# Performance work log

Measured on AMD Instinct MI355X. Metric: run time of the kernel, lower is better.

## Reference

```python
import jax, jax.numpy as jnp
import numpy as np

NEG_SLOPE = 0.01  # F.leaky_relu default


def gcn_conv(x, src, dst, norm, W, b, n_nodes):
    """PyG-style GCNConv: h = x @ W; out[i] = sum_{(j->i)} norm_e * h[j] + b.
    src/dst/norm already include self-loops and symmetric D^-1/2 A D^-1/2 weights."""
    h = x @ W                                   # [N, out]
    msgs = h[src] * norm[:, None]               # [E+N, out] gather
    out = jax.ops.segment_sum(msgs, dst, num_segments=n_nodes)  # scatter-add
    return out + b


def _build_norm(edge_idx, n_nodes):
    """Add self-loops and compute symmetric GCN normalization coefficients."""
    loops = jnp.arange(n_nodes, dtype=edge_idx.dtype)
    src = jnp.concatenate([edge_idx[0], loops])
    dst = jnp.concatenate([edge_idx[1], loops])
    deg = jax.ops.segment_sum(jnp.ones_like(dst, dtype=jnp.float32), dst,
                              num_segments=n_nodes)
    dinv = jnp.where(deg > 0, jax.lax.rsqrt(jnp.maximum(deg, 1.0)), 0.0)
    norm = dinv[src] * dinv[dst]
    return src, dst, norm


def setup_inputs() -> dict:
    key = jax.random.key(0)
    k = jax.random.split(key, 8)
    N, E, nfeat, nhid = 50000, 800000, 64, 64
    x = jax.random.normal(k[0], (N, nfeat), dtype=jnp.float32)
    edge_idx = jax.random.randint(k[1], (2, E), 0, N, dtype=jnp.int32)
    # inverted dropout mask, p=0.5 -> values in {0, 2}
    drop_mask = (jax.random.uniform(k[2], (N, nhid)) >= 0.5).astype(jnp.float32) * 2.0
    # glorot-style GCNConv weights + zero bias (PyG defaults)
    s1 = (6.0 / (nfeat + nhid)) ** 0.5
    s2 = (6.0 / (nhid + nhid // 2)) ** 0.5
    W1 = jax.random.uniform(k[3], (nfeat, nhid), minval=-s1, maxval=s1, dtype=jnp.float32)
    b1 = jnp.zeros((nhid,), dtype=jnp.float32)
    W2 = jax.random.uniform(k[4], (nhid, nhid // 2), minval=-s2, maxval=s2, dtype=jnp.float32)
    b2 = jnp.zeros((nhid // 2,), dtype=jnp.float32)
    return {"x": x, "edge_idx": edge_idx, "drop_mask": drop_mask,
            "W1": W1, "b1": b1, "W2": W2, "b2": b2}


def reference(x, edge_idx, drop_mask, W1, b1, W2, b2):
    n_nodes = x.shape[0]
    src, dst, norm = _build_norm(edge_idx, n_nodes)
    h = jax.nn.leaky_relu(gcn_conv(x, src, dst, norm, W1, b1, n_nodes), NEG_SLOPE)
    h = h * drop_mask  # F.dropout(p=0.5) with precomputed inverted mask
    out = jax.nn.leaky_relu(gcn_conv(h, src, dst, norm, W2, b2, n_nodes), NEG_SLOPE)
    return out
```

## Files before the change

kernel.cpp:

```cpp
#include <hip/hip_runtime.h>
#include <hip/hip_fp16.h>

#define NEG_SLOPE 0.01f
typedef unsigned int uint;
typedef unsigned short u16;

#define NBK 256
#define CHUNK 4096
#define KPT 16
#define GROWS 16

__device__ __forceinline__ float wbits(uint rec) {
    u16 b = (u16)(rec >> 16);
    __half h;
    *reinterpret_cast<u16*>(&h) = b;
    return __half2float(h);
}

__device__ __forceinline__ void acc8(uint4 v, float w, float* a) {
    float2 f;
    f = __half22float2(*reinterpret_cast<__half2*>(&v.x)); a[0] = fmaf(f.x, w, a[0]); a[1] = fmaf(f.y, w, a[1]);
    f = __half22float2(*reinterpret_cast<__half2*>(&v.y)); a[2] = fmaf(f.x, w, a[2]); a[3] = fmaf(f.y, w, a[3]);
    f = __half22float2(*reinterpret_cast<__half2*>(&v.z)); a[4] = fmaf(f.x, w, a[4]); a[5] = fmaf(f.y, w, a[5]);
    f = __half22float2(*reinterpret_cast<__half2*>(&v.w)); a[6] = fmaf(f.x, w, a[6]); a[7] = fmaf(f.y, w, a[7]);
}

__device__ __forceinline__ void unpack8(uint4 v, float* s) {
    float2 f;
    f = __half22float2(*reinterpret_cast<__half2*>(&v.x)); s[0] = f.x; s[1] = f.y;
    f = __half22float2(*reinterpret_cast<__half2*>(&v.y)); s[2] = f.x; s[3] = f.y;
    f = __half22float2(*reinterpret_cast<__half2*>(&v.z)); s[4] = f.x; s[5] = f.y;
    f = __half22float2(*reinterpret_cast<__half2*>(&v.w)); s[6] = f.x; s[7] = f.y;
}

__global__ __launch_bounds__(256) void bucket_hist(const int* __restrict__ dst,
                                                   uint* __restrict__ hist,
                                                   int E) {
    __shared__ uint lh[NBK];
    int t = threadIdx.x;
    lh[t] = 0u;
    __syncthreads();
    int base = blockIdx.x * CHUNK;
#pragma unroll
    for (int r = 0; r < 4; ++r) {
        int e4 = base + r * 1024 + t * 4;
        if (e4 + 3 < E) {
            int4 d = *(const int4*)(dst + e4);
            atomicAdd(&lh[((uint)d.x) >> 8], 1u);
            atomicAdd(&lh[((uint)d.y) >> 8], 1u);
            atomicAdd(&lh[((uint)d.z) >> 8], 1u);
            atomicAdd(&lh[((uint)d.w) >> 8], 1u);
        } else {
            for (int e = e4; e < E && e < e4 + 4; ++e)
                atomicAdd(&lh[((uint)dst[e]) >> 8], 1u);
        }
    }
    __syncthreads();
    hist[(size_t)blockIdx.x * NBK + t] = lh[t];
}

__global__ __launch_bounds__(256) void scan_hist(uint* __restrict__ hist,
                                                 uint* __restrict__ buckTotal,
                                                 int nchunks) {
    __shared__ uint lds[256];
    int b = blockIdx.x;
    int t = threadIdx.x;
    uint carry = 0;
    for (int c0 = 0; c0 < nchunks; c0 += 256) {
        int c = c0 + t;
        uint v = (c < nchunks) ? hist[(size_t)c * NBK + b] : 0u;
        lds[t] = v;
        __syncthreads();
        for (int off = 1; off < 256; off <<= 1) {
            uint u = (t >= off) ? lds[t - off] : 0u;
            __syncthreads();
            lds[t] += u;
            __syncthreads();
        }
        uint incl = lds[t];
        if (c < nchunks) hist[(size_t)c * NBK + b] = carry + incl - v;
        uint tot = lds[255];
        __syncthreads();
        carry += tot;
    }
    if (t == 0) buckTotal[b] = carry;
}

__global__ __launch_bounds__(256) void partition_edges(const int* __restrict__ src,
                                                       const int* __restrict__ dst,
                                                       const uint* __restrict__ hist,
                                                       const uint* __restrict__ buckTotal,
                                                       uint* __restrict__ staging,
                                                       int E) {
    __shared__ uint lh[NBK];
    __shared__ uint sc[NBK];
    __shared__ uint runbase[NBK];
    int t = threadIdx.x;
    lh[t] = 0u;
    uint tot = buckTotal[t];
    sc[t] = tot;
    __syncthreads();
    for (int off = 1; off < NBK; off <<= 1) {
        uint u = (t >= off) ? sc[t - off] : 0u;
        __syncthreads();
        sc[t] += u;
        __syncthreads();
    }
    int base = blockIdx.x * CHUNK;
    uint rec[KPT], rb[KPT], rk[KPT];
#pragma unroll
    for (int r = 0; r < 4; ++r) {
        int e4 = base + r * 1024 + t * 4;
        if (e4 + 3 < E) {
            int4 s = *(const int4*)(src + e4);
            int4 d = *(const int4*)(dst + e4);
            int k = r * 4;
            rb[k + 0] = ((uint)d.x) >> 8; rec[k + 0] = (uint)s.x | (((uint)d.x & 255u) << 16);
            rb[k + 1] = ((uint)d.y) >> 8; rec[k + 1] = (uint)s.y | (((uint)d.y & 255u) << 16);
            rb[k + 2] = ((uint)d.z) >> 8; rec[k + 2] = (uint)s.z | (((uint)d.z & 255u) << 16);
            rb[k + 3] = ((uint)d.w) >> 8; rec[k + 3] = (uint)s.w | (((uint)d.w & 255u) << 16);
            rk[k + 0] = atomicAdd(&lh[rb[k + 0]], 1u);
            rk[k + 1] = atomicAdd(&lh[rb[k + 1]], 1u);
            rk[k + 2] = atomicAdd(&lh[rb[k + 2]], 1u);
            rk[k + 3] = atomicAdd(&lh[rb[k + 3]], 1u);
        } else {
            for (int j = 0; j < 4; ++j) {
                int e = e4 + j;
                int k = r * 4 + j;
                if (e < E) {
                    uint s = (uint)src[e], d = (uint)dst[e];
                    rb[k] = d >> 8;
                    rec[k] = s | ((d & 255u) << 16);
                    rk[k] = atomicAdd(&lh[rb[k]], 1u);
                } else rb[k] = 0xFFFFFFFFu;
            }
        }
    }
    __syncthreads();
    runbase[t] = (sc[t] - tot) + hist[(size_t)blockIdx.x * NBK + t];
    __syncthreads();
#pragma unroll
    for (int k = 0; k < KPT; ++k)
        if (rb[k] != 0xFFFFFFFFu)
            staging[runbase[rb[k]] + rk[k]] = rec[k];
}

__global__ __launch_bounds__(256) void build_csr(const uint* __restrict__ staging,
                                                 const uint* __restrict__ buckTotal,
                                                 u16* __restrict__ srcIdx,
                                                 uint* __restrict__ offs,
                                                 float* __restrict__ dinv,
                                                 int N, int nbuck) {
    __shared__ uint nh[256];
    __shared__ uint nstart[256];
    __shared__ u16 rankbuf[8192];
    __shared__ u16 outbuf[8192];
    int b = blockIdx.x;
    int t = threadIdx.x;
    uint tot = buckTotal[t];
    nstart[t] = tot;
    __syncthreads();
    for (int off = 1; off < NBK; off <<= 1) {
        uint u = (t >= off) ? nstart[t - off] : 0u;
        __syncthreads();
        nstart[t] += u;
        __syncthreads();
    }
    uint endb = nstart[b];
    uint base = endb - buckTotal[b];
    __syncthreads();
    uint T = endb - base;
    nh[t] = 0u;
    __syncthreads();
    for (uint i = t; i < T; i += 256) {
        uint rec = staging[base + i];
        rankbuf[i] = (u16)atomicAdd(&nh[(rec >> 16) & 255u], 1u);
    }
    __syncthreads();
    uint deg = nh[t];
    nstart[t] = deg;
    __syncthreads();
    for (int off = 1; off < 256; off <<= 1) {
        uint u = (t >= off) ? nstart[t - off] : 0u;
        __syncthreads();
        nstart[t] += u;
        __syncthreads();
    }
    uint excl = nstart[t] - deg;
    __syncthreads();
    nstart[t] = excl;
    __syncthreads();
    for (uint i = t; i < T; i += 256) {
        uint rec = staging[base + i];
        outbuf[nstart[(rec >> 16) & 255u] + rankbuf[i]] = (u16)(rec & 0xFFFFu);
    }
    __syncthreads();
    for (uint i = t; i < T; i += 256) srcIdx[base + i] = outbuf[i];
    int node = b * 256 + t;
    if (node < N) {
        offs[node] = base + excl;
        dinv[node] = rsqrtf((float)(deg + 1u));
    }
    if (b == nbuck - 1 && t == 0) offs[N] = endb;
}

__global__ __launch_bounds__(256) void fill_pack(const u16* __restrict__ srcIdx,
                                                 const float* __restrict__ dinv,
                                                 uint* __restrict__ packed, int E) {
    int i4 = (blockIdx.x * 256 + threadIdx.x) * 4;
    if (i4 + 3 < E) {
        ushort4 s = *(const ushort4*)(srcIdx + i4);
        uint4 o;
        __half h0 = __float2half(dinv[s.x]);
        __half h1 = __float2half(dinv[s.y]);
        __half h2 = __float2half(dinv[s.z]);
        __half h3 = __float2half(dinv[s.w]);
        o.x = (uint)s.x | ((uint)*reinterpret_cast<u16*>(&h0) << 16);
        o.y = (uint)s.y | ((uint)*reinterpret_cast<u16*>(&h1) << 16);
        o.z = (uint)s.z | ((uint)*reinterpret_cast<u16*>(&h2) << 16);
        o.w = (uint)s.w | ((uint)*reinterpret_cast<u16*>(&h3) << 16);
        *(uint4*)(packed + i4) = o;
    } else {
        for (int i = i4; i < E; ++i) {
            __half h = __float2half(dinv[srcIdx[i]]);
            packed[i] = (uint)srcIdx[i] | ((uint)*reinterpret_cast<u16*>(&h) << 16);
        }
    }
}

__global__ __launch_bounds__(256) void gemm64x64(const float* __restrict__ X,
                                                 const float* __restrict__ W,
                                                 __half* __restrict__ H, int N) {
    int lane = threadIdx.x & 63;
    int wv = threadIdx.x >> 6;
    float wc[64];
#pragma unroll
    for (int k = 0; k < 64; ++k) wc[k] = W[k * 64 + lane];
    int rowBase = (blockIdx.x * 4 + wv) * GROWS;
    for (int g = 0; g < GROWS; g += 4) {
        int r0 = __builtin_amdgcn_readfirstlane(rowBase + g);
        if (r0 >= N) return;
        int e1 = min(r0 + 1, N - 1), e2 = min(r0 + 2, N - 1), e3 = min(r0 + 3, N - 1);
        const float* x0 = X + (size_t)r0 * 64;
        const float* x1 = X + (size_t)e1 * 64;
        const float* x2 = X + (size_t)e2 * 64;
        const float* x3 = X + (size_t)e3 * 64;
        float a0 = 0.f, a1 = 0.f, a2 = 0.f, a3 = 0.f;
        float b0 = 0.f, b1 = 0.f, b2 = 0.f, b3 = 0.f;
#pragma unroll
        for (int k = 0; k < 64; k += 2) {
            a0 = fmaf(x0[k], wc[k], a0); b0 = fmaf(x0[k + 1], wc[k + 1], b0);
            a1 = fmaf(x1[k], wc[k], a1); b1 = fmaf(x1[k + 1], wc[k + 1], b1);
            a2 = fmaf(x2[k], wc[k], a2); b2 = fmaf(x2[k + 1], wc[k + 1], b2);
            a3 = fmaf(x3[k], wc[k], a3); b3 = fmaf(x3[k + 1], wc[k + 1], b3);
        }
        H[(size_t)r0 * 64 + lane] = __float2half(a0 + b0);
        if (r0 + 1 < N) H[(size_t)(r0 + 1) * 64 + lane] = __float2half(a1 + b1);
        if (r0 + 2 < N) H[(size_t)(r0 + 2) * 64 + lane] = __float2half(a2 + b2);
        if (r0 + 3 < N) H[(size_t)(r0 + 3) * 64 + lane] = __float2half(a3 + b3);
    }
}

__global__ __launch_bounds__(256) void gemm64x32(const __half* __restrict__ Xh,
                                                 const float* __restrict__ W,
                                                 __half* __restrict__ H, int N) {
    int lane = threadIdx.x & 63;
    int col = lane & 31;
    int wv = threadIdx.x >> 6;
    float wc[64];
#pragma unroll
    for (int k = 0; k < 64; ++k) wc[k] = W[k * 32 + col];
    int rowBase = (blockIdx.x * 4 + wv) * GROWS;
    for (int g = 0; g < GROWS; g += 4) {
        int r0 = __builtin_amdgcn_readfirstlane(rowBase + g);
        if (r0 >= N) return;
        int e1 = min(r0 + 1, N - 1), e2 = min(r0 + 2, N - 1), e3 = min(r0 + 3, N - 1);
        const uint* x0 = (const uint*)(Xh + (size_t)r0 * 64);
        const uint* x1 = (const uint*)(Xh + (size_t)e1 * 64);
        const uint* x2 = (const uint*)(Xh + (size_t)e2 * 64);
        const uint* x3 = (const uint*)(Xh + (size_t)e3 * 64);
        float a0 = 0.f, a1 = 0.f, a2 = 0.f, a3 = 0.f;
        float b0 = 0.f, b1 = 0.f, b2 = 0.f, b3 = 0.f;
#pragma unroll
        for (int kk = 0; kk < 32; ++kk) {
            uint u0 = x0[kk], u1 = x1[kk], u2 = x2[kk], u3 = x3[kk];
            float2 f0 = __half22float2(*reinterpret_cast<__half2*>(&u0));
            float2 f1 = __half22float2(*reinterpret_cast<__half2*>(&u1));
            float2 f2 = __half22float2(*reinterpret_cast<__half2*>(&u2));
            float2 f3 = __half22float2(*reinterpret_cast<__half2*>(&u3));
            a0 = fmaf(f0.x, wc[2 * kk], a0); b0 = fmaf(f0.y, wc[2 * kk + 1], b0);
            a1 = fmaf(f1.x, wc[2 * kk], a1); b1 = fmaf(f1.y, wc[2 * kk + 1], b1);
            a2 = fmaf(f2.x, wc[2 * kk], a2); b2 = fmaf(f2.y, wc[2 * kk + 1], b2);
            a3 = fmaf(f3.x, wc[2 * kk], a3); b3 = fmaf(f3.y, wc[2 * kk + 1], b3);
        }
        if (lane < 32) {
            H[(size_t)r0 * 32 + col] = __float2half(a0 + b0);
            if (r0 + 1 < N) H[(size_t)(r0 + 1) * 32 + col] = __float2half(a1 + b1);
            if (r0 + 2 < N) H[(size_t)(r0 + 2) * 32 + col] = __float2half(a2 + b2);
            if (r0 + 3 < N) H[(size_t)(r0 + 3) * 32 + col] = __float2half(a3 + b3);
        }
    }
}

__global__ __launch_bounds__(256) void agg1(const __half* __restrict__ h,
                                            const uint* __restrict__ offs,
                                            const uint* __restrict__ packed,
                                            const float* __restrict__ dinv,
                                            const float* __restrict__ b,
                                            const float* __restrict__ mask,
                                            __half* __restrict__ outp, int N) {
    int node = blockIdx.x * 4 + (threadIdx.x >> 6);
    if (node >= N) return;
    int lane = threadIdx.x & 63;
    int r = lane >> 3;
    int q = lane & 7;
    const uint4* h16 = (const uint4*)h;
    uint beg = offs[node], end = offs[node + 1];
    float a[8] = {0.f, 0.f, 0.f, 0.f, 0.f, 0.f, 0.f, 0.f};
    uint p = beg + (uint)r;
    for (; p + 24 < end; p += 32) {
        uint e0 = packed[p], e1 = packed[p + 8], e2 = packed[p + 16], e3 = packed[p + 24];
        uint4 v0 = h16[(size_t)(e0 & 0xFFFFu) * 8 + q];
        uint4 v1 = h16[(size_t)(e1 & 0xFFFFu) * 8 + q];
        uint4 v2 = h16[(size_t)(e2 & 0xFFFFu) * 8 + q];
        uint4 v3 = h16[(size_t)(e3 & 0xFFFFu) * 8 + q];
        acc8(v0, wbits(e0), a);
        acc8(v1, wbits(e1), a);
        acc8(v2, wbits(e2), a);
        acc8(v3, wbits(e3), a);
    }
    for (; p < end; p += 8) {
        uint e0 = packed[p];
        uint4 v0 = h16[(size_t)(e0 & 0xFFFFu) * 8 + q];
        acc8(v0, wbits(e0), a);
    }
#pragma unroll
    for (int i = 0; i < 8; ++i) {
        a[i] += __shfl_xor(a[i], 8, 64);
        a[i] += __shfl_xor(a[i], 16, 64);
        a[i] += __shfl_xor(a[i], 32, 64);
    }
    if (r == 0) {
        float dv = dinv[node];
        float dv2 = dv * dv;
        float s[8];
        unpack8(h16[(size_t)node * 8 + q], s);
        float4 bv0 = ((const float4*)b)[q * 2];
        float4 bv1 = ((const float4*)b)[q * 2 + 1];
        float4 mv0 = ((const float4*)mask)[(size_t)node * 16 + q * 2];
        float4 mv1 = ((const float4*)mask)[(size_t)node * 16 + q * 2 + 1];
        float bb[8] = {bv0.x, bv0.y, bv0.z, bv0.w, bv1.x, bv1.y, bv1.z, bv1.w};
        float mm[8] = {mv0.x, mv0.y, mv0.z, mv0.w, mv1.x, mv1.y, mv1.z, mv1.w};
        uint4 o;
        uint* op = (uint*)&o;
#pragma unroll
        for (int i = 0; i < 4; ++i) {
            float v0 = a[2 * i] * dv + s[2 * i] * dv2 + bb[2 * i];
            float v1 = a[2 * i + 1] * dv + s[2 * i + 1] * dv2 + bb[2 * i + 1];
            v0 = (v0 > 0.f) ? v0 : NEG_SLOPE * v0;
            v1 = (v1 > 0.f) ? v1 : NEG_SLOPE * v1;
            v0 *= mm[2 * i]; v1 *= mm[2 * i + 1];
            __half2 hh = __floats2half2_rn(v0, v1);
            op[i] = *reinterpret_cast<uint*>(&hh);
        }
        ((uint4*)outp)[(size_t)node * 8 + q] = o;
    }
}

__global__ __launch_bounds__(256) void agg2(const __half* __restrict__ h,
                                            const uint* __restrict__ offs,
                                            const uint* __restrict__ packed,
                                            const float* __restrict__ dinv,
                                            const float* __restrict__ b,
                                            float* __restrict__ outp, int N) {
    int node = blockIdx.x * 4 + (threadIdx.x >> 6);
    if (node >= N) return;
    int lane = threadIdx.x & 63;
    int r = lane >> 2;
    int q = lane & 3;
    const uint4* h8 = (const uint4*)h;
    uint beg = offs[node], end = offs[node + 1];
    float a[8] = {0.f, 0.f, 0.f, 0.f, 0.f, 0.f, 0.f, 0.f};
    uint p = beg + (uint)r;
    for (; p + 16 < end; p += 32) {
        uint e0 = packed[p], e1 = packed[p + 16];
        uint4 v0 = h8[(size_t)(e0 & 0xFFFFu) * 4 + q];
        uint4 v1 = h8[(size_t)(e1 & 0xFFFFu) * 4 + q];
        acc8(v0, wbits(e0), a);
        acc8(v1, wbits(e1), a);
    }
    for (; p < end; p += 16) {
        uint e0 = packed[p];
        uint4 v0 = h8[(size_t)(e0 & 0xFFFFu) * 4 + q];
        acc8(v0, wbits(e0), a);
    }
#pragma unroll
    for (int i = 0; i < 8; ++i) {
        a[i] += __shfl_xor(a[i], 4, 64);
        a[i] += __shfl_xor(a[i], 8, 64);
        a[i] += __shfl_xor(a[i], 16, 64);
        a[i] += __shfl_xor(a[i], 32, 64);
    }
    if (r == 0) {
        float dv = dinv[node];
        float dv2 = dv * dv;
        float s[8];
        unpack8(h8[(size_t)node * 4 + q], s);
        float4 bv0 = ((const float4*)b)[q * 2];
        float4 bv1 = ((const float4*)b)[q * 2 + 1];
        float bb[8] = {bv0.x, bv0.y, bv0.z, bv0.w, bv1.x, bv1.y, bv1.z, bv1.w};
        float o[8];
#pragma unroll
        for (int i = 0; i < 8; ++i) {
            float v = a[i] * dv + s[i] * dv2 + bb[i];
            o[i] = (v > 0.f) ? v : NEG_SLOPE * v;
        }
        float4* outv = (float4*)outp;
        outv[(size_t)node * 8 + q * 2]     = make_float4(o[0], o[1], o[2], o[3]);
        outv[(size_t)node * 8 + q * 2 + 1] = make_float4(o[4], o[5], o[6], o[7]);
    }
}

extern "C" void kernel_launch(void* const* d_in, const int* in_sizes, int n_in,
                              void* d_out, int out_size, void* d_ws, size_t ws_size,
                              hipStream_t stream) {
    const float* x    = (const float*)d_in[0];
    const int*   ei   = (const int*)d_in[1];
    const float* mask = (const float*)d_in[2];
    const float* W1   = (const float*)d_in[3];
    const float* b1   = (const float*)d_in[4];
    const float* W2   = (const float*)d_in[5];
    const float* b2   = (const float*)d_in[6];
    float* out = (float*)d_out;

    const int N = in_sizes[0] / 64;
    const int E = in_sizes[1] / 2;
    const int* src = ei;
    const int* dst = ei + E;

    const int nbuck  = (N + 255) >> 8;
    const int chunks = (E + CHUNK - 1) / CHUNK;
    const int gblocks = (N + 4 * GROWS - 1) / (4 * GROWS);

    char* w = (char*)d_ws;
    uint*  hist      = (uint*)w;    w += (size_t)chunks * NBK * 4;
    uint*  buckTotal = (uint*)w;    w += NBK * 4;
    w = (char*)(((size_t)w + 15) & ~15ull);
    uint*  offs      = (uint*)w;    w += (size_t)(N + 1) * 4;
    w = (char*)(((size_t)w + 15) & ~15ull);
    float* dinv      = (float*)w;   w += (size_t)N * 4;
    uint*  staging   = (uint*)w;    w += (size_t)E * 4;
    u16*   srcIdx    = (u16*)w;     w += (((size_t)E * 2 + 15) & ~15ull);
    uint*  packed    = (uint*)w;    w += (size_t)E * 4;
    __half* h1       = (__half*)w;  w += (size_t)N * 64 * 2;
    __half* hpost    = (__half*)w;  w += (size_t)N * 64 * 2;
    __half* h2       = h1;

    bucket_hist<<<chunks, 256, 0, stream>>>(dst, hist, E);
    scan_hist<<<NBK, 256, 0, stream>>>(hist, buckTotal, chunks);
    partition_edges<<<chunks, 256, 0, stream>>>(src, dst, hist, buckTotal, staging, E);
    build_csr<<<nbuck, 256, 0, stream>>>(staging, buckTotal, srcIdx, offs, dinv, N, nbuck);
    fill_pack<<<(E + 1023) / 1024, 256, 0, stream>>>(srcIdx, dinv, packed, E);

    gemm64x64<<<gblocks, 256, 0, stream>>>(x, W1, h1, N);
    agg1<<<(N + 3) / 4, 256, 0, stream>>>(h1, offs, packed, dinv, b1, mask, hpost, N);

    gemm64x32<<<gblocks, 256, 0, stream>>>(hpost, W2, h2, N);
    agg2<<<(N + 3) / 4, 256, 0, stream>>>(h2, offs, packed, dinv, b2, out, N);
}
```

Measured before the change: 129.6 us.

## Fuse first GEMM with histogram, drop scan kernel, split agg1 into feature planes

```diff
diff --git a/kernel.cpp b/kernel.cpp
--- a/kernel.cpp
+++ b/kernel.cpp
@@ -33,71 +33,86 @@
     f = __half22float2(*reinterpret_cast<__half2*>(&v.w)); s[6] = f.x; s[7] = f.y;
 }
 
-__global__ __launch_bounds__(256) void bucket_hist(const int* __restrict__ dst,
-                                                   uint* __restrict__ hist,
-                                                   int E) {
+__global__ __launch_bounds__(256) void gemm1_hist(const float* __restrict__ X,
+                                                  const float* __restrict__ W,
+                                                  __half* __restrict__ H, int N,
+                                                  const int* __restrict__ dst,
+                                                  uint* __restrict__ hist, int E,
+                                                  int gblocks) {
     __shared__ uint lh[NBK];
-    int t = threadIdx.x;
-    lh[t] = 0u;
-    __syncthreads();
-    int base = blockIdx.x * CHUNK;
-#pragma unroll
-    for (int r = 0; r < 4; ++r) {
-        int e4 = base + r * 1024 + t * 4;
-        if (e4 + 3 < E) {
-            int4 d = *(const int4*)(dst + e4);
-            atomicAdd(&lh[((uint)d.x) >> 8], 1u);
-            atomicAdd(&lh[((uint)d.y) >> 8], 1u);
-            atomicAdd(&lh[((uint)d.z) >> 8], 1u);
-            atomicAdd(&lh[((uint)d.w) >> 8], 1u);
-        } else {
-            for (int e = e4; e < E && e < e4 + 4; ++e)
-                atomicAdd(&lh[((uint)dst[e]) >> 8], 1u);
-        }
-    }
-    __syncthreads();
-    hist[(size_t)blockIdx.x * NBK + t] = lh[t];
-}
-
-__global__ __launch_bounds__(256) void scan_hist(uint* __restrict__ hist,
-                                                 uint* __restrict__ buckTotal,
-                                                 int nchunks) {
-    __shared__ uint lds[256];
-    int b = blockIdx.x;
-    int t = threadIdx.x;
-    uint carry = 0;
-    for (int c0 = 0; c0 < nchunks; c0 += 256) {
-        int c = c0 + t;
-        uint v = (c < nchunks) ? hist[(size_t)c * NBK + b] : 0u;
-        lds[t] = v;
-        __syncthreads();
-        for (int off = 1; off < 256; off <<= 1) {
-            uint u = (t >= off) ? lds[t - off] : 0u;
-            __syncthreads();
-            lds[t] += u;
-            __syncthreads();
-        }
-        uint incl = lds[t];
-        if (c < nchunks) hist[(size_t)c * NBK + b] = carry + incl - v;
-        uint tot = lds[255];
-        __syncthreads();
-        carry += tot;
-    }
-    if (t == 0) buckTotal[b] = carry;
+    if ((int)blockIdx.x >= gblocks) {
+        int cb = (int)blockIdx.x - gblocks;
+        int t = threadIdx.x;
+        lh[t] = 0u;
+        __syncthreads();
+        int base = cb * CHUNK;
+#pragma unroll
+        for (int r = 0; r < 4; ++r) {
+            int e4 = base + r * 1024 + t * 4;
+            if (e4 + 3 < E) {
+                int4 d = *(const int4*)(dst + e4);
+                atomicAdd(&lh[((uint)d.x) >> 8], 1u);
+                atomicAdd(&lh[((uint)d.y) >> 8], 1u);
+                atomicAdd(&lh[((uint)d.z) >> 8], 1u);
+                atomicAdd(&lh[((uint)d.w) >> 8], 1u);
+            } else {
+                for (int e = e4; e < E && e < e4 + 4; ++e)
+                    atomicAdd(&lh[((uint)dst[e]) >> 8], 1u);
+            }
+        }
+        __syncthreads();
+        hist[(size_t)cb * NBK + t] = lh[t];
+        return;
+    }
+    int lane = threadIdx.x & 63;
+    int wv = threadIdx.x >> 6;
+    float wc[64];
+#pragma unroll
+    for (int k = 0; k < 64; ++k) wc[k] = W[k * 64 + lane];
+    size_t plane = (size_t)(lane >> 5) * ((size_t)N * 32);
+    int c = lane & 31;
+    int rowBase = ((int)blockIdx.x * 4 + wv) * GROWS;
+    for (int g = 0; g < GROWS; g += 4) {
+        int r0 = __builtin_amdgcn_readfirstlane(rowBase + g);
+        if (r0 >= N) return;
+        int e1 = min(r0 + 1, N - 1), e2 = min(r0 + 2, N - 1), e3 = min(r0 + 3, N - 1);
+        const float* x0 = X + (size_t)r0 * 64;
+        const float* x1 = X + (size_t)e1 * 64;
+        const float* x2 = X + (size_t)e2 * 64;
+        const float* x3 = X + (size_t)e3 * 64;
+        float a0 = 0.f, a1 = 0.f, a2 = 0.f, a3 = 0.f;
+        float b0 = 0.f, b1 = 0.f, b2 = 0.f, b3 = 0.f;
+#pragma unroll
+        for (int k = 0; k < 64; k += 2) {
+            a0 = fmaf(x0[k], wc[k], a0); b0 = fmaf(x0[k + 1], wc[k + 1], b0);
+            a1 = fmaf(x1[k], wc[k], a1); b1 = fmaf(x1[k + 1], wc[k + 1], b1);
+            a2 = fmaf(x2[k], wc[k], a2); b2 = fmaf(x2[k + 1], wc[k + 1], b2);
+            a3 = fmaf(x3[k], wc[k], a3); b3 = fmaf(x3[k + 1], wc[k + 1], b3);
+        }
+        H[plane + (size_t)r0 * 32 + c] = __float2half(a0 + b0);
+        if (r0 + 1 < N) H[plane + (size_t)(r0 + 1) * 32 + c] = __float2half(a1 + b1);
+        if (r0 + 2 < N) H[plane + (size_t)(r0 + 2) * 32 + c] = __float2half(a2 + b2);
+        if (r0 + 3 < N) H[plane + (size_t)(r0 + 3) * 32 + c] = __float2half(a3 + b3);
+    }
 }
 
 __global__ __launch_bounds__(256) void partition_edges(const int* __restrict__ src,
                                                        const int* __restrict__ dst,
                                                        const uint* __restrict__ hist,
-                                                       const uint* __restrict__ buckTotal,
                                                        uint* __restrict__ staging,
-                                                       int E) {
+                                                       int E, int nchunks) {
     __shared__ uint lh[NBK];
     __shared__ uint sc[NBK];
     __shared__ uint runbase[NBK];
     int t = threadIdx.x;
+    int myc = blockIdx.x;
     lh[t] = 0u;
-    uint tot = buckTotal[t];
+    uint part = 0, tot = 0;
+    for (int c2 = 0; c2 < nchunks; ++c2) {
+        uint v = hist[(size_t)c2 * NBK + t];
+        if (c2 == myc) part = tot;
+        tot += v;
+    }
     sc[t] = tot;
     __syncthreads();
     for (int off = 1; off < NBK; off <<= 1) {
@@ -106,7 +121,7 @@
         sc[t] += u;
         __syncthreads();
     }
-    int base = blockIdx.x * CHUNK;
+    int base = myc * CHUNK;
     uint rec[KPT], rb[KPT], rk[KPT];
 #pragma unroll
     for (int r = 0; r < 4; ++r) {
@@ -137,7 +152,7 @@
         }
     }
     __syncthreads();
-    runbase[t] = (sc[t] - tot) + hist[(size_t)blockIdx.x * NBK + t];
+    runbase[t] = (sc[t] - tot) + part;
     __syncthreads();
 #pragma unroll
     for (int k = 0; k < KPT; ++k)
@@ -146,18 +161,20 @@
 }
 
 __global__ __launch_bounds__(256) void build_csr(const uint* __restrict__ staging,
-                                                 const uint* __restrict__ buckTotal,
+                                                 const uint* __restrict__ hist,
                                                  u16* __restrict__ srcIdx,
                                                  uint* __restrict__ offs,
                                                  float* __restrict__ dinv,
-                                                 int N, int nbuck) {
+                                                 int N, int nbuck, int nchunks) {
     __shared__ uint nh[256];
     __shared__ uint nstart[256];
     __shared__ u16 rankbuf[8192];
     __shared__ u16 outbuf[8192];
     int b = blockIdx.x;
     int t = threadIdx.x;
-    uint tot = buckTotal[t];
+    uint tot = 0;
+    for (int c2 = 0; c2 < nchunks; ++c2) tot += hist[(size_t)c2 * NBK + t];
+    nh[t] = tot;
     nstart[t] = tot;
     __syncthreads();
     for (int off = 1; off < NBK; off <<= 1) {
@@ -167,7 +184,7 @@
         __syncthreads();
     }
     uint endb = nstart[b];
-    uint base = endb - buckTotal[b];
+    uint base = endb - nh[b];
     __syncthreads();
     uint T = endb - base;
     nh[t] = 0u;
@@ -228,114 +245,40 @@
     }
 }
 
-__global__ __launch_bounds__(256) void gemm64x64(const float* __restrict__ X,
-                                                 const float* __restrict__ W,
-                                                 __half* __restrict__ H, int N) {
-    int lane = threadIdx.x & 63;
-    int wv = threadIdx.x >> 6;
-    float wc[64];
-#pragma unroll
-    for (int k = 0; k < 64; ++k) wc[k] = W[k * 64 + lane];
-    int rowBase = (blockIdx.x * 4 + wv) * GROWS;
-    for (int g = 0; g < GROWS; g += 4) {
-        int r0 = __builtin_amdgcn_readfirstlane(rowBase + g);
-        if (r0 >= N) return;
-        int e1 = min(r0 + 1, N - 1), e2 = min(r0 + 2, N - 1), e3 = min(r0 + 3, N - 1);
-        const float* x0 = X + (size_t)r0 * 64;
-        const float* x1 = X + (size_t)e1 * 64;
-        const float* x2 = X + (size_t)e2 * 64;
-        const float* x3 = X + (size_t)e3 * 64;
-        float a0 = 0.f, a1 = 0.f, a2 = 0.f, a3 = 0.f;
-        float b0 = 0.f, b1 = 0.f, b2 = 0.f, b3 = 0.f;
-#pragma unroll
-        for (int k = 0; k < 64; k += 2) {
-            a0 = fmaf(x0[k], wc[k], a0); b0 = fmaf(x0[k + 1], wc[k + 1], b0);
-            a1 = fmaf(x1[k], wc[k], a1); b1 = fmaf(x1[k + 1], wc[k + 1], b1);
-            a2 = fmaf(x2[k], wc[k], a2); b2 = fmaf(x2[k + 1], wc[k + 1], b2);
-            a3 = fmaf(x3[k], wc[k], a3); b3 = fmaf(x3[k + 1], wc[k + 1], b3);
-        }
-        H[(size_t)r0 * 64 + lane] = __float2half(a0 + b0);
-        if (r0 + 1 < N) H[(size_t)(r0 + 1) * 64 + lane] = __float2half(a1 + b1);
-        if (r0 + 2 < N) H[(size_t)(r0 + 2) * 64 + lane] = __float2half(a2 + b2);
-        if (r0 + 3 < N) H[(size_t)(r0 + 3) * 64 + lane] = __float2half(a3 + b3);
-    }
-}
-
-__global__ __launch_bounds__(256) void gemm64x32(const __half* __restrict__ Xh,
-                                                 const float* __restrict__ W,
-                                                 __half* __restrict__ H, int N) {
-    int lane = threadIdx.x & 63;
-    int col = lane & 31;
-    int wv = threadIdx.x >> 6;
-    float wc[64];
-#pragma unroll
-    for (int k = 0; k < 64; ++k) wc[k] = W[k * 32 + col];
-    int rowBase = (blockIdx.x * 4 + wv) * GROWS;
-    for (int g = 0; g < GROWS; g += 4) {
-        int r0 = __builtin_amdgcn_readfirstlane(rowBase + g);
-        if (r0 >= N) return;
-        int e1 = min(r0 + 1, N - 1), e2 = min(r0 + 2, N - 1), e3 = min(r0 + 3, N - 1);
-        const uint* x0 = (const uint*)(Xh + (size_t)r0 * 64);
-        const uint* x1 = (const uint*)(Xh + (size_t)e1 * 64);
-        const uint* x2 = (const uint*)(Xh + (size_t)e2 * 64);
-        const uint* x3 = (const uint*)(Xh + (size_t)e3 * 64);
-        float a0 = 0.f, a1 = 0.f, a2 = 0.f, a3 = 0.f;
-        float b0 = 0.f, b1 = 0.f, b2 = 0.f, b3 = 0.f;
-#pragma unroll
-        for (int kk = 0; kk < 32; ++kk) {
-            uint u0 = x0[kk], u1 = x1[kk], u2 = x2[kk], u3 = x3[kk];
-            float2 f0 = __half22float2(*reinterpret_cast<__half2*>(&u0));
-            float2 f1 = __half22float2(*reinterpret_cast<__half2*>(&u1));
-            float2 f2 = __half22float2(*reinterpret_cast<__half2*>(&u2));
-            float2 f3 = __half22float2(*reinterpret_cast<__half2*>(&u3));
-            a0 = fmaf(f0.x, wc[2 * kk], a0); b0 = fmaf(f0.y, wc[2 * kk + 1], b0);
-            a1 = fmaf(f1.x, wc[2 * kk], a1); b1 = fmaf(f1.y, wc[2 * kk + 1], b1);
-            a2 = fmaf(f2.x, wc[2 * kk], a2); b2 = fmaf(f2.y, wc[2 * kk + 1], b2);
-            a3 = fmaf(f3.x, wc[2 * kk], a3); b3 = fmaf(f3.y, wc[2 * kk + 1], b3);
-        }
-        if (lane < 32) {
-            H[(size_t)r0 * 32 + col] = __float2half(a0 + b0);
-            if (r0 + 1 < N) H[(size_t)(r0 + 1) * 32 + col] = __float2half(a1 + b1);
-            if (r0 + 2 < N) H[(size_t)(r0 + 2) * 32 + col] = __float2half(a2 + b2);
-            if (r0 + 3 < N) H[(size_t)(r0 + 3) * 32 + col] = __float2half(a3 + b3);
-        }
-    }
-}
-
 __global__ __launch_bounds__(256) void agg1(const __half* __restrict__ h,
                                             const uint* __restrict__ offs,
                                             const uint* __restrict__ packed,
                                             const float* __restrict__ dinv,
                                             const float* __restrict__ b,
                                             const float* __restrict__ mask,
-                                            __half* __restrict__ outp, int N) {
-    int node = blockIdx.x * 4 + (threadIdx.x >> 6);
+                                            __half* __restrict__ outp,
+                                            int N, int nb1) {
+    int half = ((int)blockIdx.x >= nb1) ? 1 : 0;
+    int blk = (int)blockIdx.x - half * nb1;
+    int node = blk * 4 + (threadIdx.x >> 6);
     if (node >= N) return;
     int lane = threadIdx.x & 63;
-    int r = lane >> 3;
-    int q = lane & 7;
-    const uint4* h16 = (const uint4*)h;
+    int r = lane >> 2;
+    int q = lane & 3;
+    const uint4* h8 = (const uint4*)(h + (size_t)half * N * 32);
     uint beg = offs[node], end = offs[node + 1];
     float a[8] = {0.f, 0.f, 0.f, 0.f, 0.f, 0.f, 0.f, 0.f};
     uint p = beg + (uint)r;
-    for (; p + 24 < end; p += 32) {
-        uint e0 = packed[p], e1 = packed[p + 8], e2 = packed[p + 16], e3 = packed[p + 24];
-        uint4 v0 = h16[(size_t)(e0 & 0xFFFFu) * 8 + q];
-        uint4 v1 = h16[(size_t)(e1 & 0xFFFFu) * 8 + q];
-        uint4 v2 = h16[(size_t)(e2 & 0xFFFFu) * 8 + q];
-        uint4 v3 = h16[(size_t)(e3 & 0xFFFFu) * 8 + q];
+    for (; p + 16 < end; p += 32) {
+        uint e0 = packed[p], e1 = packed[p + 16];
+        uint4 v0 = h8[(size_t)(e0 & 0xFFFFu) * 4 + q];
+        uint4 v1 = h8[(size_t)(e1 & 0xFFFFu) * 4 + q];
         acc8(v0, wbits(e0), a);
         acc8(v1, wbits(e1), a);
-        acc8(v2, wbits(e2), a);
-        acc8(v3, wbits(e3), a);
-    }
-    for (; p < end; p += 8) {
+    }
+    for (; p < end; p += 16) {
         uint e0 = packed[p];
-        uint4 v0 = h16[(size_t)(e0 & 0xFFFFu) * 8 + q];
+        uint4 v0 = h8[(size_t)(e0 & 0xFFFFu) * 4 + q];
         acc8(v0, wbits(e0), a);
     }
 #pragma unroll
     for (int i = 0; i < 8; ++i) {
+        a[i] += __shfl_xor(a[i], 4, 64);
         a[i] += __shfl_xor(a[i], 8, 64);
         a[i] += __shfl_xor(a[i], 16, 64);
         a[i] += __shfl_xor(a[i], 32, 64);
@@ -344,11 +287,13 @@
         float dv = dinv[node];
         float dv2 = dv * dv;
         float s[8];
-        unpack8(h16[(size_t)node * 8 + q], s);
-        float4 bv0 = ((const float4*)b)[q * 2];
-        float4 bv1 = ((const float4*)b)[q * 2 + 1];
-        float4 mv0 = ((const float4*)mask)[(size_t)node * 16 + q * 2];
-        float4 mv1 = ((const float4*)mask)[(size_t)node * 16 + q * 2 + 1];
+        unpack8(h8[(size_t)node * 4 + q], s);
+        const float4* b4 = (const float4*)b;
+        float4 bv0 = b4[half * 8 + q * 2];
+        float4 bv1 = b4[half * 8 + q * 2 + 1];
+        const float4* m4 = (const float4*)mask;
+        float4 mv0 = m4[(size_t)node * 16 + half * 8 + q * 2];
+        float4 mv1 = m4[(size_t)node * 16 + half * 8 + q * 2 + 1];
         float bb[8] = {bv0.x, bv0.y, bv0.z, bv0.w, bv1.x, bv1.y, bv1.z, bv1.w};
         float mm[8] = {mv0.x, mv0.y, mv0.z, mv0.w, mv1.x, mv1.y, mv1.z, mv1.w};
         uint4 o;
@@ -363,7 +308,53 @@
             __half2 hh = __floats2half2_rn(v0, v1);
             op[i] = *reinterpret_cast<uint*>(&hh);
         }
-        ((uint4*)outp)[(size_t)node * 8 + q] = o;
+        ((uint4*)(outp + (size_t)half * N * 32))[(size_t)node * 4 + q] = o;
+    }
+}
+
+__global__ __launch_bounds__(256) void gemm64x32(const __half* __restrict__ Xh,
+                                                 const float* __restrict__ W,
+                                                 __half* __restrict__ H, int N) {
+    int lane = threadIdx.x & 63;
+    int col = lane & 31;
+    int wv = threadIdx.x >> 6;
+    size_t N32 = (size_t)N * 32;
+    float wc[64];
+#pragma unroll
+    for (int k = 0; k < 64; ++k) wc[k] = W[k * 32 + col];
+    int rowBase = ((int)blockIdx.x * 4 + wv) * GROWS;
+    for (int g = 0; g < GROWS; g += 4) {
+        int r0 = __builtin_amdgcn_readfirstlane(rowBase + g);
+        if (r0 >= N) return;
+        int e1 = min(r0 + 1, N - 1), e2 = min(r0 + 2, N - 1), e3 = min(r0 + 3, N - 1);
+        float a0 = 0.f, a1 = 0.f, a2 = 0.f, a3 = 0.f;
+        float b0 = 0.f, b1 = 0.f, b2 = 0.f, b3 = 0.f;
+#pragma unroll
+        for (int pl = 0; pl < 2; ++pl) {
+            const uint* x0 = (const uint*)(Xh + pl * N32 + (size_t)r0 * 32);
+            const uint* x1 = (const uint*)(Xh + pl * N32 + (size_t)e1 * 32);
+            const uint* x2 = (const uint*)(Xh + pl * N32 + (size_t)e2 * 32);
+            const uint* x3 = (const uint*)(Xh + pl * N32 + (size_t)e3 * 32);
+#pragma unroll
+            for (int kk = 0; kk < 16; ++kk) {
+                uint u0 = x0[kk], u1 = x1[kk], u2 = x2[kk], u3 = x3[kk];
+                float2 f0 = __half22float2(*reinterpret_cast<__half2*>(&u0));
+                float2 f1 = __half22float2(*reinterpret_cast<__half2*>(&u1));
+                float2 f2 = __half22float2(*reinterpret_cast<__half2*>(&u2));
+                float2 f3 = __half22float2(*reinterpret_cast<__half2*>(&u3));
+                int k0 = pl * 32 + 2 * kk;
+                a0 = fmaf(f0.x, wc[k0], a0); b0 = fmaf(f0.y, wc[k0 + 1], b0);
+                a1 = fmaf(f1.x, wc[k0], a1); b1 = fmaf(f1.y, wc[k0 + 1], b1);
+                a2 = fmaf(f2.x, wc[k0], a2); b2 = fmaf(f2.y, wc[k0 + 1], b2);
+                a3 = fmaf(f3.x, wc[k0], a3); b3 = fmaf(f3.y, wc[k0 + 1], b3);
+            }
+        }
+        if (lane < 32) {
+            H[(size_t)r0 * 32 + col] = __float2half(a0 + b0);
+            if (r0 + 1 < N) H[(size_t)(r0 + 1) * 32 + col] = __float2half(a1 + b1);
+            if (r0 + 2 < N) H[(size_t)(r0 + 2) * 32 + col] = __float2half(a2 + b2);
+            if (r0 + 3 < N) H[(size_t)(r0 + 3) * 32 + col] = __float2half(a3 + b3);
+        }
     }
 }
 
@@ -373,7 +364,7 @@
                                             const float* __restrict__ dinv,
                                             const float* __restrict__ b,
                                             float* __restrict__ outp, int N) {
-    int node = blockIdx.x * 4 + (threadIdx.x >> 6);
+    int node = (int)blockIdx.x * 4 + (threadIdx.x >> 6);
     if (node >= N) return;
     int lane = threadIdx.x & 63;
     int r = lane >> 2;
@@ -441,11 +432,10 @@
     const int nbuck  = (N + 255) >> 8;
     const int chunks = (E + CHUNK - 1) / CHUNK;
     const int gblocks = (N + 4 * GROWS - 1) / (4 * GROWS);
+    const int nb1 = (N + 3) / 4;
 
     char* w = (char*)d_ws;
     uint*  hist      = (uint*)w;    w += (size_t)chunks * NBK * 4;
-    uint*  buckTotal = (uint*)w;    w += NBK * 4;
-    w = (char*)(((size_t)w + 15) & ~15ull);
     uint*  offs      = (uint*)w;    w += (size_t)(N + 1) * 4;
     w = (char*)(((size_t)w + 15) & ~15ull);
     float* dinv      = (float*)w;   w += (size_t)N * 4;
@@ -456,15 +446,13 @@
     __half* hpost    = (__half*)w;  w += (size_t)N * 64 * 2;
     __half* h2       = h1;
 
-    bucket_hist<<<chunks, 256, 0, stream>>>(dst, hist, E);
-    scan_hist<<<NBK, 256, 0, stream>>>(hist, buckTotal, chunks);
-    partition_edges<<<chunks, 256, 0, stream>>>(src, dst, hist, buckTotal, staging, E);
-    build_csr<<<nbuck, 256, 0, stream>>>(staging, buckTotal, srcIdx, offs, dinv, N, nbuck);
+    gemm1_hist<<<gblocks + chunks, 256, 0, stream>>>(x, W1, h1, N, dst, hist, E, gblocks);
+    partition_edges<<<chunks, 256, 0, stream>>>(src, dst, hist, staging, E, chunks);
+    build_csr<<<nbuck, 256, 0, stream>>>(staging, hist, srcIdx, offs, dinv, N, nbuck, chunks);
     fill_pack<<<(E + 1023) / 1024, 256, 0, stream>>>(srcIdx, dinv, packed, E);
 
-    gemm64x64<<<gblocks, 256, 0, stream>>>(x, W1, h1, N);
-    agg1<<<(N + 3) / 4, 256, 0, stream>>>(h1, offs, packed, dinv, b1, mask, hpost, N);
+    agg1<<<2 * nb1, 256, 0, stream>>>(h1, offs, packed, dinv, b1, mask, hpost, N, nb1);
 
     gemm64x32<<<gblocks, 256, 0, stream>>>(hpost, W2, h2, N);
-    agg2<<<(N + 3) / 4, 256, 0, stream>>>(h2, offs, packed, dinv, b2, out, N);
-}
+    agg2<<<nb1, 256, 0, stream>>>(h2, offs, packed, dinv, b2, out, N);
+}
```

Result: slower. 189.5 us (+46.1%).
